# Performance work log

Hardware: AMD Instinct MI355X
Metric: run time of the kernel (lower is better)

## Reference

```python
import jax, jax.numpy as jnp
import numpy as np

D_MODEL = 1024
N_HEADS = 16
D_K = D_MODEL // N_HEADS
D_FF = 4096
THETA = 10000.0
B, S = 2, 2048
EPS = 1e-5


def _trunc_normal(key, shape, fan_in, fan_out):
    std = np.sqrt(2.0 / (fan_in + fan_out))
    return std * jax.random.truncated_normal(key, -3.0, 3.0, shape, dtype=jnp.float32)


def setup_inputs() -> dict:
    key = jax.random.key(0)
    ks = jax.random.split(key, 9)
    x = jax.random.normal(ks[0], (B, S, D_MODEL), dtype=jnp.float32)
    wq = _trunc_normal(ks[1], (D_MODEL, D_MODEL), D_MODEL, D_MODEL)
    wk = _trunc_normal(ks[2], (D_MODEL, D_MODEL), D_MODEL, D_MODEL)
    wv = _trunc_normal(ks[3], (D_MODEL, D_MODEL), D_MODEL, D_MODEL)
    wo = _trunc_normal(ks[4], (D_MODEL, D_MODEL), D_MODEL, D_MODEL)
    w1 = _trunc_normal(ks[5], (D_FF, D_MODEL), D_MODEL, D_FF)
    w2 = _trunc_normal(ks[6], (D_MODEL, D_FF), D_FF, D_MODEL)
    w3 = _trunc_normal(ks[7], (D_FF, D_MODEL), D_MODEL, D_FF)
    g1 = jnp.ones((D_MODEL,), dtype=jnp.float32)
    g2 = jnp.ones((D_MODEL,), dtype=jnp.float32)
    return {"x": x, "wq": wq, "wk": wk, "wv": wv, "wo": wo,
            "w1": w1, "w2": w2, "w3": w3, "g1": g1, "g2": g2}


def _rmsnorm(x, gain):
    xf = x.astype(jnp.float32)
    rms = jnp.sqrt(jnp.mean(xf * xf, axis=-1, keepdims=True) + EPS)
    return (xf / rms * gain).astype(x.dtype)


def _rope(x):
    # x: [B, H, S, D_K]; block-diag 2x2 rotations on consecutive pairs
    s, d = x.shape[-2], x.shape[-1]
    pos = jnp.arange(s, dtype=jnp.float32)  # [S]
    k = jnp.arange(d // 2, dtype=jnp.float32)
    ang = pos[:, None] / (THETA ** (2.0 * k / d))[None, :]  # [S, d/2]
    cos, sin = jnp.cos(ang), jnp.sin(ang)
    xp = x.reshape(*x.shape[:-1], d // 2, 2)
    x0, x1 = xp[..., 0], xp[..., 1]
    r0 = cos * x0 - sin * x1
    r1 = sin * x0 + cos * x1
    return jnp.stack([r0, r1], axis=-1).reshape(x.shape)


def reference(x, wq, wk, wv, wo, w1, w2, w3, g1, g2):
    # --- attention sublayer ---
    h = _rmsnorm(x, g1)
    q = h @ wq.T
    k = h @ wk.T
    v = h @ wv.T
    def split_heads(t):
        b, s, _ = t.shape
        return t.reshape(b, s, N_HEADS, D_K).transpose(0, 2, 1, 3)  # [B,H,S,Dk]
    q, k, v = split_heads(q), split_heads(k), split_heads(v)
    q, k = _rope(q), _rope(k)
    scores = jnp.einsum('bhqd,bhkd->bhqk', q, k) / jnp.sqrt(jnp.float32(D_K))
    s = x.shape[-2]
    causal = jnp.tril(jnp.ones((s, s), dtype=bool))
    scores = jnp.where(causal, scores, -jnp.inf)
    attn = jax.nn.softmax(scores, axis=-1)
    o = jnp.einsum('bhqk,bhkd->bhqd', attn, v)
    o = o.transpose(0, 2, 1, 3).reshape(x.shape[0], s, D_MODEL)
    x = x + o @ wo.T
    # --- SwiGLU FFN sublayer ---
    h2 = _rmsnorm(x, g2)
    a = h2 @ w1.T
    gate = a * jax.nn.sigmoid(a)
    ff = (gate * (h2 @ w3.T)) @ w2.T
    return x + ff
```

## Files before the change

### kernel.cpp

```cpp
#include <hip/hip_runtime.h>
#include <hip/hip_bf16.h>
#include <cstddef>
#include <cstdint>

#define D_MODEL 1024
#define N_HEADS 16
#define D_K     64
#define D_FF    4096
#define BATCH   2
#define SEQ     2048
#define TOKENS  (BATCH * SEQ)
#define EPS     1e-5f

typedef __attribute__((ext_vector_type(8))) short short8;
typedef __attribute__((ext_vector_type(4))) float f32x4;

#define MFMA_BF16 __builtin_amdgcn_mfma_f32_16x16x32_bf16

static __device__ __forceinline__ short f2bf(float f) {
    __hip_bfloat16 h = __float2bfloat16(f);
    short s;
    __builtin_memcpy(&s, &h, 2);
    return s;
}
static __device__ __forceinline__ float bf2f(short s) {
    __hip_bfloat16 h;
    __builtin_memcpy(&h, &s, 2);
    return __bfloat162float(h);
}

static __device__ __forceinline__ void async_ld16(const short* g, short* l) {
    __builtin_amdgcn_global_load_lds(
        (const __attribute__((address_space(1))) void*)g,
        (__attribute__((address_space(3))) void*)l,
        16, 0, 0);
}

__global__ __launch_bounds__(256) void prep_kernel(
    const float* wq, const float* wk, const float* wv, const float* wo,
    const float* w1, const float* w3, const float* w2, short* dst,
    const float* x, const float* g1, __hip_bfloat16* h)
{
    if (blockIdx.x < 16384) {
        const size_t M1 = 1 << 20;
        size_t e = ((size_t)blockIdx.x * 256 + threadIdx.x) * 4;
        const float* src;
        size_t off;
        if (e < M1)            { src = wq; off = e; }
        else if (e < 2 * M1)   { src = wk; off = e - M1; }
        else if (e < 3 * M1)   { src = wv; off = e - 2 * M1; }
        else if (e < 4 * M1)   { src = wo; off = e - 3 * M1; }
        else if (e < 12 * M1) {
            size_t r = (e - 4 * M1) >> 10;
            size_t col = e & 1023;
            size_t p = r >> 5, half = (r >> 4) & 1, idx = r & 15;
            src = half ? w3 : w1;
            off = (p * 16 + idx) * 1024 + col;
        }
        else                   { src = w2; off = e - 12 * M1; }
        float4 v = *reinterpret_cast<const float4*>(src + off);
        short4 o;
        o.x = f2bf(v.x); o.y = f2bf(v.y); o.z = f2bf(v.z); o.w = f2bf(v.w);
        *reinterpret_cast<short4*>(dst + e) = o;
    } else {
        int row = blockIdx.x - 16384;
        int tid = threadIdx.x;
        int lane = tid & 63, wave = tid >> 6;
        const float4* xv = reinterpret_cast<const float4*>(x + (size_t)row * D_MODEL);
        float4 v = xv[tid];
        float ss = v.x * v.x + v.y * v.y + v.z * v.z + v.w * v.w;
#pragma unroll
        for (int m = 1; m < 64; m <<= 1) ss += __shfl_xor(ss, m, 64);
        __shared__ float red[4];
        if (lane == 0) red[wave] = ss;
        __syncthreads();
        float tot = red[0] + red[1] + red[2] + red[3];
        float inv = 1.0f / sqrtf(tot * (1.0f / D_MODEL) + EPS);
        float4 gv = reinterpret_cast<const float4*>(g1)[tid];
        size_t base = (size_t)row * D_MODEL + (size_t)tid * 4;
        h[base + 0] = __float2bfloat16(v.x * inv * gv.x);
        h[base + 1] = __float2bfloat16(v.y * inv * gv.y);
        h[base + 2] = __float2bfloat16(v.z * inv * gv.z);
        h[base + 3] = __float2bfloat16(v.w * inv * gv.w);
    }
}

__global__ __launch_bounds__(256) void resid_norm_kernel(
    const float* __restrict__ x, const short* __restrict__ P,
    const float* __restrict__ g, float* __restrict__ out,
    __hip_bfloat16* __restrict__ h)
{
    int row = blockIdx.x;
    int tid = threadIdx.x;
    int lane = tid & 63, wave = tid >> 6;
    size_t base = (size_t)row * D_MODEL + (size_t)tid * 4;
    float4 v = *reinterpret_cast<const float4*>(x + base);
    short4 p0 = *reinterpret_cast<const short4*>(P + base);
    short4 p1 = *reinterpret_cast<const short4*>(P + (size_t)TOKENS * D_MODEL + base);
    v.x += bf2f(p0.x) + bf2f(p1.x); v.y += bf2f(p0.y) + bf2f(p1.y);
    v.z += bf2f(p0.z) + bf2f(p1.z); v.w += bf2f(p0.w) + bf2f(p1.w);
    *reinterpret_cast<float4*>(out + base) = v;
    float ss = v.x * v.x + v.y * v.y + v.z * v.z + v.w * v.w;
#pragma unroll
    for (int m = 1; m < 64; m <<= 1) ss += __shfl_xor(ss, m, 64);
    __shared__ float red[4];
    if (lane == 0) red[wave] = ss;
    __syncthreads();
    float tot = red[0] + red[1] + red[2] + red[3];
    float inv = 1.0f / sqrtf(tot * (1.0f / D_MODEL) + EPS);
    float4 gv = reinterpret_cast<const float4*>(g)[tid];
    h[base + 0] = __float2bfloat16(v.x * inv * gv.x);
    h[base + 1] = __float2bfloat16(v.y * inv * gv.y);
    h[base + 2] = __float2bfloat16(v.z * inv * gv.z);
    h[base + 3] = __float2bfloat16(v.w * inv * gv.w);
}

__global__ __launch_bounds__(256) void final_add_kernel(
    float* __restrict__ out, const short* __restrict__ Q)
{
    size_t base = ((size_t)blockIdx.x * 256 + threadIdx.x) * 4;
    float4 v = *reinterpret_cast<const float4*>(out + base);
    short4 q0 = *reinterpret_cast<const short4*>(Q + base);
    short4 q1 = *reinterpret_cast<const short4*>(Q + (size_t)TOKENS * D_MODEL + base);
    v.x += bf2f(q0.x) + bf2f(q1.x); v.y += bf2f(q0.y) + bf2f(q1.y);
    v.z += bf2f(q0.z) + bf2f(q1.z); v.w += bf2f(q0.w) + bf2f(q1.w);
    *reinterpret_cast<float4*>(out + base) = v;
}

template<int EPI>
__global__ __launch_bounds__(256) void gemm_bt(
    const short* __restrict__ A, const short* __restrict__ W,
    void* __restrict__ Cout, int K, int lda, int ldc)
{
    __shared__ short Alds[128 * 64];
    __shared__ short Blds[128 * 64];

    const int lane = threadIdx.x & 63;
    const int wv = threadIdx.x >> 6;
    const int quad = lane >> 4, l16 = lane & 15;
    const int wm = wv & 1, wn = wv >> 1;
    const int rowblk = blockIdx.y * 128;
    const int colblk = blockIdx.x * 128;

    const int srow = lane >> 2;
    const int sseg = ((lane & 3) - (lane >> 3)) & 3;
    const short* sA0 = A + (size_t)(rowblk + wv * 16 + srow) * lda + sseg * 8;
    const short* sA1 = A + (size_t)(rowblk + (wv + 4) * 16 + srow) * lda + sseg * 8;
    const short* sB0 = W + (size_t)(colblk + wv * 16 + srow) * (size_t)K + sseg * 8;
    const short* sB1 = W + (size_t)(colblk + (wv + 4) * 16 + srow) * (size_t)K + sseg * 8;
    short* lA0 = &Alds[wv * 512];
    short* lA1 = &Alds[(wv + 4) * 512];
    short* lB0 = &Blds[wv * 512];
    short* lB1 = &Blds[(wv + 4) * 512];

    int aoff[4], boff[4];
#pragma unroll
    for (int i = 0; i < 4; ++i) {
        int tr = wm * 64 + i * 16 + l16;
        aoff[i] = tr * 32 + ((quad + (tr >> 1)) & 3) * 8;
        int tc = wn * 64 + i * 16 + l16;
        boff[i] = tc * 32 + ((quad + (tc >> 1)) & 3) * 8;
    }

    f32x4 acc[4][4];
#pragma unroll
    for (int i = 0; i < 4; ++i)
#pragma unroll
        for (int j = 0; j < 4; ++j)
            acc[i][j] = (f32x4){0.f, 0.f, 0.f, 0.f};

    for (int kk = 0; kk < K; kk += 64) {
        if (kk) __syncthreads();
        async_ld16(sA0 + kk, lA0);
        async_ld16(sA1 + kk, lA1);
        async_ld16(sB0 + kk, lB0);
        async_ld16(sB1 + kk, lB1);
        async_ld16(sA0 + kk + 32, lA0 + 4096);
        async_ld16(sA1 + kk + 32, lA1 + 4096);
        async_ld16(sB0 + kk + 32, lB0 + 4096);
        async_ld16(sB1 + kk + 32, lB1 + 4096);
        __syncthreads();
#pragma unroll
        for (int hf = 0; hf < 2; ++hf) {
            short8 af[4], bf[4];
#pragma unroll
            for (int i = 0; i < 4; ++i)
                af[i] = *reinterpret_cast<const short8*>(&Alds[hf * 4096 + aoff[i]]);
#pragma unroll
            for (int j = 0; j < 4; ++j)
                bf[j] = *reinterpret_cast<const short8*>(&Blds[hf * 4096 + boff[j]]);
#pragma unroll
            for (int i = 0; i < 4; ++i)
#pragma unroll
                for (int j = 0; j < 4; ++j)
                    acc[i][j] = MFMA_BF16(af[i], bf[j], acc[i][j], 0, 0, 0);
        }
    }

    if (EPI == 2) {
#pragma unroll
        for (int i = 0; i < 4; ++i) {
#pragma unroll
            for (int jp = 0; jp < 2; ++jp) {
#pragma unroll
                for (int r = 0; r < 4; ++r) {
                    int row = rowblk + wm * 64 + i * 16 + quad * 4 + r;
                    int col = blockIdx.x * 64 + wn * 32 + jp * 16 + l16;
                    float a = acc[i][2 * jp][r];
                    float b3 = acc[i][2 * jp + 1][r];
                    float gv = a / (1.f + __expf(-a)) * b3;
                    reinterpret_cast<__hip_bfloat16*>(Cout)[(size_t)row * ldc + col] =
                        __float2bfloat16(gv);
                }
            }
        }
    } else {
#pragma unroll
        for (int i = 0; i < 4; ++i) {
#pragma unroll
            for (int j = 0; j < 4; ++j) {
#pragma unroll
                for (int r = 0; r < 4; ++r) {
                    int row = rowblk + wm * 64 + i * 16 + quad * 4 + r;
                    int col = colblk + wn * 64 + j * 16 + l16;
                    size_t idx = (size_t)row * ldc + col;
                    if (EPI == 3)
                        reinterpret_cast<__hip_bfloat16*>(Cout)[idx] =
                            __float2bfloat16(acc[i][j][r]);
                    else
                        reinterpret_cast<float*>(Cout)[idx] = acc[i][j][r];
                }
            }
        }
    }
}

template<int SPLIT>
__global__ __launch_bounds__(256) void gemm_bt_sk(
    const short* __restrict__ A, const short* __restrict__ W,
    short* __restrict__ P, int K, int lda, int ldc)
{
    __shared__ short Alds[128 * 64];
    __shared__ short Blds[128 * 64];

    const int Kc = K / SPLIT;
    const int kbase = blockIdx.z * Kc;
    short* Cout = P + (size_t)blockIdx.z * TOKENS * ldc;

    const int lane = threadIdx.x & 63;
    const int wv = threadIdx.x >> 6;
    const int quad = lane >> 4, l16 = lane & 15;
    const int wm = wv & 1, wn = wv >> 1;
    const int rowblk = blockIdx.y * 128;
    const int colblk = blockIdx.x * 128;

    const int srow = lane >> 2;
    const int sseg = ((lane & 3) - (lane >> 3)) & 3;
    const short* sA0 = A + (size_t)(rowblk + wv * 16 + srow) * lda + kbase + sseg * 8;
    const short* sA1 = A + (size_t)(rowblk + (wv + 4) * 16 + srow) * lda + kbase + sseg * 8;
    const short* sB0 = W + (size_t)(colblk + wv * 16 + srow) * (size_t)K + kbase + sseg * 8;
    const short* sB1 = W + (size_t)(colblk + (wv + 4) * 16 + srow) * (size_t)K + kbase + sseg * 8;
    short* lA0 = &Alds[wv * 512];
    short* lA1 = &Alds[(wv + 4) * 512];
    short* lB0 = &Blds[wv * 512];
    short* lB1 = &Blds[(wv + 4) * 512];

    int aoff[4], boff[4];
#pragma unroll
    for (int i = 0; i < 4; ++i) {
        int tr = wm * 64 + i * 16 + l16;
        aoff[i] = tr * 32 + ((quad + (tr >> 1)) & 3) * 8;
        int tc = wn * 64 + i * 16 + l16;
        boff[i] = tc * 32 + ((quad + (tc >> 1)) & 3) * 8;
    }

    f32x4 acc[4][4];
#pragma unroll
    for (int i = 0; i < 4; ++i)
#pragma unroll
        for (int j = 0; j < 4; ++j)
            acc[i][j] = (f32x4){0.f, 0.f, 0.f, 0.f};

    for (int kk = 0; kk < Kc; kk += 64) {
        if (kk) __syncthreads();
        async_ld16(sA0 + kk, lA0);
        async_ld16(sA1 + kk, lA1);
        async_ld16(sB0 + kk, lB0);
        async_ld16(sB1 + kk, lB1);
        async_ld16(sA0 + kk + 32, lA0 + 4096);
        async_ld16(sA1 + kk + 32, lA1 + 4096);
        async_ld16(sB0 + kk + 32, lB0 + 4096);
        async_ld16(sB1 + kk + 32, lB1 + 4096);
        __syncthreads();
#pragma unroll
        for (int hf = 0; hf < 2; ++hf) {
            short8 af[4], bf[4];
#pragma unroll
            for (int i = 0; i < 4; ++i)
                af[i] = *reinterpret_cast<const short8*>(&Alds[hf * 4096 + aoff[i]]);
#pragma unroll
            for (int j = 0; j < 4; ++j)
                bf[j] = *reinterpret_cast<const short8*>(&Blds[hf * 4096 + boff[j]]);
#pragma unroll
            for (int i = 0; i < 4; ++i)
#pragma unroll
                for (int j = 0; j < 4; ++j)
                    acc[i][j] = MFMA_BF16(af[i], bf[j], acc[i][j], 0, 0, 0);
        }
    }

#pragma unroll
    for (int i = 0; i < 4; ++i) {
#pragma unroll
        for (int j = 0; j < 4; ++j) {
#pragma unroll
            for (int r = 0; r < 4; ++r) {
                int row = rowblk + wm * 64 + i * 16 + quad * 4 + r;
                int col = colblk + wn * 64 + j * 16 + l16;
                Cout[(size_t)row * ldc + col] = f2bf(acc[i][j][r]);
            }
        }
    }
}

__global__ __launch_bounds__(256) void qkv_post_kernel(
    const short* __restrict__ qk,
    __hip_bfloat16* __restrict__ qb, __hip_bfloat16* __restrict__ kb,
    __hip_bfloat16* __restrict__ vt)
{
    __shared__ float tile[64 * 65];
    if (blockIdx.x < 8192) {
        int idx = blockIdx.x * 256 + threadIdx.x;
        int p = idx & 31;
        int h = (idx >> 5) & 15;
        int tok = idx >> 9;
        int s = tok & (SEQ - 1);
        int b = tok >> 11;
        float invf = exp2f((float)p * -(0.03125f * 13.287712379549449f));
        float ang = (float)s * invf;
        float c, sn;
        sincosf(ang, &sn, &c);
        size_t base = (size_t)tok * 3072 + h * 64 + 2 * p;
        float q0 = bf2f(qk[base]),           q1 = bf2f(qk[base + 1]);
        float k0 = bf2f(qk[base + D_MODEL]), k1 = bf2f(qk[base + D_MODEL + 1]);
        float cq = c * 0.125f, sq = sn * 0.125f;
        size_t ob = ((size_t)(b * N_HEADS + h) * SEQ + s) * D_K + 2 * p;
        qb[ob]     = __float2bfloat16(cq * q0 - sq * q1);
        qb[ob + 1] = __float2bfloat16(sq * q0 + cq * q1);
        kb[ob]     = __float2bfloat16(c * k0 - sn * k1);
        kb[ob + 1] = __float2bfloat16(sn * k0 + c * k1);
    } else {
        int bid = blockIdx.x - 8192;
        const int bh = bid >> 5;
        const int s0 = (bid & 31) * 64;
        const int t = threadIdx.x;
        const int r = t >> 4, c4 = (t & 15) * 4;
        const short* src = qk + ((size_t)(bh >> 4) * SEQ + s0) * 3072 + 2048 + (bh & 15) * 64;
#pragma unroll
        for (int p = 0; p < 4; ++p) {
            int s = p * 16 + r;
            short4 v = *reinterpret_cast<const short4*>(src + (size_t)s * 3072 + c4);
            tile[s * 65 + c4 + 0] = bf2f(v.x);
            tile[s * 65 + c4 + 1] = bf2f(v.y);
            tile[s * 65 + c4 + 2] = bf2f(v.z);
            tile[s * 65 + c4 + 3] = bf2f(v.w);
        }
        __syncthreads();
        const int d = t >> 2, sg = (t & 3) * 16;
        __hip_bfloat16* dst = vt + ((size_t)bh * 64 + d) * SEQ + s0 + sg;
        short8 o0, o1;
#pragma unroll
        for (int i = 0; i < 8; ++i) o0[i] = f2bf(tile[(sg + i) * 65 + d]);
#pragma unroll
        for (int i = 0; i < 8; ++i) o1[i] = f2bf(tile[(sg + 8 + i) * 65 + d]);
        *reinterpret_cast<short8*>(dst) = o0;
        *reinterpret_cast<short8*>(dst + 8) = o1;
    }
}

__global__ __launch_bounds__(512) void attn_kernel(
    const __hip_bfloat16* __restrict__ qbp, const __hip_bfloat16* __restrict__ kbp,
    const __hip_bfloat16* __restrict__ vtp, __hip_bfloat16* __restrict__ o)
{
    const int wave = threadIdx.x >> 6;
    const int lane = threadIdx.x & 63;
    const int quad = lane >> 4, l16 = lane & 15;
    const int bh = blockIdx.y;
    const int qt = (wave < 4) ? blockIdx.x : (15 - blockIdx.x);
    const int q0 = qt * 128 + (wave & 3) * 32;
    const int qmax = q0 + 31;

    const short* Q  = reinterpret_cast<const short*>(qbp) + ((size_t)bh * SEQ + q0) * D_K;
    const short* Kg = reinterpret_cast<const short*>(kbp) + (size_t)bh * SEQ * D_K;
    const short* Vg = reinterpret_cast<const short*>(vtp) + (size_t)bh * D_K * SEQ;

    short8 qfr[2][2];
#pragma unroll
    for (int f = 0; f < 2; ++f) {
        qfr[f][0] = *reinterpret_cast<const short8*>(Q + (size_t)(f * 16 + l16) * D_K + quad * 8);
        qfr[f][1] = *reinterpret_cast<const short8*>(Q + (size_t)(f * 16 + l16) * D_K + 32 + quad * 8);
    }

    f32x4 oacc[2][4];
    f32x4 lacc[2];
#pragma unroll
    for (int f = 0; f < 2; ++f) {
        lacc[f] = (f32x4){0.f, 0.f, 0.f, 0.f};
#pragma unroll
        for (int g = 0; g < 4; ++g) oacc[f][g] = (f32x4){0.f, 0.f, 0.f, 0.f};
    }

    short8 ones;
#pragma unroll
    for (int i = 0; i < 8; ++i) ones[i] = (short)0x3F80;

    __shared__ short Kt[64 * 64];
    __shared__ short Vl[64 * 64];
    __shared__ short plds[8][32 * 72];
    short* myP = &plds[wave][0];

    const int srl = lane >> 3;
    const int sp  = lane & 7;
    const int strow = wave * 8 + srl;
    const int sl = (sp - strow) & 7;

    const int ntile = 2 * (15 - blockIdx.x) + 2;
    for (int tile = 0; tile < ntile; ++tile) {
        const int kb0 = tile * 64;
        if (tile) __syncthreads();
        async_ld16(Kg + (size_t)(kb0 + strow) * D_K + sl * 8, &Kt[wave * 512]);
        async_ld16(Vg + (size_t)strow * SEQ + kb0 + sl * 8, &Vl[wave * 512]);
        __syncthreads();

        if (kb0 <= qmax) {
            f32x4 sf[2][4];
#pragma unroll
            for (int kg = 0; kg < 4; ++kg) {
                int row = kg * 16 + l16;
                const short* kr = &Kt[row * 64];
                short8 kf0 = *reinterpret_cast<const short8*>(&kr[((quad + row) & 7) * 8]);
                short8 kf1 = *reinterpret_cast<const short8*>(&kr[((quad + 4 + row) & 7) * 8]);
#pragma unroll
                for (int f = 0; f < 2; ++f) {
                    f32x4 z = (f32x4){0.f, 0.f, 0.f, 0.f};
                    z = MFMA_BF16(qfr[f][0], kf0, z, 0, 0, 0);
                    z = MFMA_BF16(qfr[f][1], kf1, z, 0, 0, 0);
                    sf[f][kg] = z;
                }
            }
#pragma unroll
            for (int f = 0; f < 2; ++f) {
                const int qlo = q0 + f * 16;
#pragma unroll
                for (int kg = 0; kg < 4; ++kg) {
                    const int keylo = kb0 + kg * 16;
                    const bool needmask = keylo >= qlo;
                    const int key = keylo + l16;
#pragma unroll
                    for (int r = 0; r < 4; ++r) {
                        float p = __expf(sf[f][kg][r]);
                        if (needmask) {
                            int qrow = qlo + quad * 4 + r;
                            p = (key > qrow) ? 0.f : p;
                        }
                        myP[(f * 16 + quad * 4 + r) * 72 + kg * 16 + l16] = f2bf(p);
                    }
                }
            }
            asm volatile("s_waitcnt lgkmcnt(0)" ::: "memory");
            short8 pf[2][2];
#pragma unroll
            for (int f = 0; f < 2; ++f) {
#pragma unroll
                for (int hh = 0; hh < 2; ++hh) {
                    pf[f][hh] = *reinterpret_cast<const short8*>(
                        &myP[(f * 16 + l16) * 72 + (hh * 4 + quad) * 8]);
                    lacc[f] = MFMA_BF16(pf[f][hh], ones, lacc[f], 0, 0, 0);
                }
            }
#pragma unroll
            for (int g = 0; g < 4; ++g) {
                int rd = g * 16 + l16;
                const short* vr = &Vl[rd * 64];
                short8 vf0 = *reinterpret_cast<const short8*>(&vr[((quad + rd) & 7) * 8]);
                short8 vf1 = *reinterpret_cast<const short8*>(&vr[((quad + 4 + rd) & 7) * 8]);
#pragma unroll
                for (int f = 0; f < 2; ++f) {
                    oacc[f][g] = MFMA_BF16(pf[f][0], vf0, oacc[f][g], 0, 0, 0);
                    oacc[f][g] = MFMA_BF16(pf[f][1], vf1, oacc[f][g], 0, 0, 0);
                }
            }
        }
    }

    const int b = bh >> 4, h = bh & 15;
#pragma unroll
    for (int f = 0; f < 2; ++f) {
#pragma unroll
        for (int g = 0; g < 4; ++g) {
#pragma unroll
            for (int r = 0; r < 4; ++r) {
                int qrow = q0 + f * 16 + quad * 4 + r;
                float v = oacc[f][g][r] / lacc[f][r];
                o[(size_t)(b * SEQ + qrow) * D_MODEL + h * 64 + g * 16 + l16] =
                    __float2bfloat16(v);
            }
        }
    }
}

extern "C" void kernel_launch(void* const* d_in, const int* in_sizes, int n_in,
                              void* d_out, int out_size, void* d_ws, size_t ws_size,
                              hipStream_t stream)
{
    const float* x  = (const float*)d_in[0];
    const float* wq = (const float*)d_in[1];
    const float* wk = (const float*)d_in[2];
    const float* wv = (const float*)d_in[3];
    const float* wo = (const float*)d_in[4];
    const float* w1 = (const float*)d_in[5];
    const float* w2 = (const float*)d_in[6];
    const float* w3 = (const float*)d_in[7];
    const float* g1 = (const float*)d_in[8];
    const float* g2 = (const float*)d_in[9];
    float* out = (float*)d_out;

    char* ws = (char*)d_ws;
    const size_t OFF_WTS  = 0;
    const size_t OFF_H    = 33554432;
    const size_t OFF_QKV  = 41943040;
    const size_t OFF_QB   = 92274688;
    const size_t OFF_KB   = 100663296;
    const size_t OFF_VT   = 109051904;
    const size_t OFF_O    = 117440512;
    const size_t OFF_P    = OFF_QKV;
    const size_t OFF_GATE = OFF_QKV;
    const size_t OFF_Q2   = OFF_QB;

    short* wts  = (short*)(ws + OFF_WTS);
    short* wqkvb = wts;
    short* wob  = wts + (size_t)3 * (1 << 20);
    short* w13b = wts + (size_t)4 * (1 << 20);
    short* w2b  = wts + (size_t)12 * (1 << 20);
    __hip_bfloat16* h  = (__hip_bfloat16*)(ws + OFF_H);
    short* qkvb = (short*)(ws + OFF_QKV);
    __hip_bfloat16* qb = (__hip_bfloat16*)(ws + OFF_QB);
    __hip_bfloat16* kb = (__hip_bfloat16*)(ws + OFF_KB);
    __hip_bfloat16* vt = (__hip_bfloat16*)(ws + OFF_VT);
    __hip_bfloat16* ob = (__hip_bfloat16*)(ws + OFF_O);
    short* Pwo  = (short*)(ws + OFF_P);
    __hip_bfloat16* gate = (__hip_bfloat16*)(ws + OFF_GATE);
    short* Qw2  = (short*)(ws + OFF_Q2);

    prep_kernel<<<20480, 256, 0, stream>>>(wq, wk, wv, wo, w1, w3, w2, wts, x, g1, h);
    gemm_bt<3><<<dim3(3072 / 128, TOKENS / 128), 256, 0, stream>>>(
        (const short*)h, wqkvb, qkvb, D_MODEL, D_MODEL, 3072);
    qkv_post_kernel<<<9216, 256, 0, stream>>>(qkvb, qb, kb, vt);
    attn_kernel<<<dim3(8, BATCH * N_HEADS), 512, 0, stream>>>(qb, kb, vt, ob);
    gemm_bt_sk<2><<<dim3(D_MODEL / 128, TOKENS / 128, 2), 256, 0, stream>>>(
        (const short*)ob, wob, Pwo, D_MODEL, D_MODEL, D_MODEL);
    resid_norm_kernel<<<TOKENS, 256, 0, stream>>>(x, Pwo, g2, out, h);
    gemm_bt<2><<<dim3(8192 / 128, TOKENS / 128), 256, 0, stream>>>(
        (const short*)h, w13b, gate, D_MODEL, D_MODEL, D_FF);
    gemm_bt_sk<2><<<dim3(D_MODEL / 128, TOKENS / 128, 2), 256, 0, stream>>>(
        (const short*)gate, w2b, Qw2, D_FF, D_FF, D_MODEL);
    final_add_kernel<<<TOKENS * D_MODEL / 1024, 256, 0, stream>>>(out, Qw2);
    (void)in_sizes; (void)n_in; (void)out_size; (void)ws_size;
}
```

Baseline: 377.4 us.

## Shrink attention blocks to two waves and raise split-K for W2 GEMM

```diff
diff --git a/kernel.cpp b/kernel.cpp
--- a/kernel.cpp
+++ b/kernel.cpp
@@ -120,10 +120,13 @@
 {
     size_t base = ((size_t)blockIdx.x * 256 + threadIdx.x) * 4;
     float4 v = *reinterpret_cast<const float4*>(out + base);
-    short4 q0 = *reinterpret_cast<const short4*>(Q + base);
-    short4 q1 = *reinterpret_cast<const short4*>(Q + (size_t)TOKENS * D_MODEL + base);
-    v.x += bf2f(q0.x) + bf2f(q1.x); v.y += bf2f(q0.y) + bf2f(q1.y);
-    v.z += bf2f(q0.z) + bf2f(q1.z); v.w += bf2f(q0.w) + bf2f(q1.w);
+#pragma unroll
+    for (int z = 0; z < 4; ++z) {
+        short4 q = *reinterpret_cast<const short4*>(
+            Q + (size_t)z * TOKENS * D_MODEL + base);
+        v.x += bf2f(q.x); v.y += bf2f(q.y);
+        v.z += bf2f(q.z); v.w += bf2f(q.w);
+    }
     *reinterpret_cast<float4*>(out + base) = v;
 }
 
@@ -378,7 +381,7 @@
     }
 }
 
-__global__ __launch_bounds__(512) void attn_kernel(
+__global__ __launch_bounds__(128) void attn_kernel(
     const __hip_bfloat16* __restrict__ qbp, const __hip_bfloat16* __restrict__ kbp,
     const __hip_bfloat16* __restrict__ vtp, __hip_bfloat16* __restrict__ o)
 {
@@ -386,8 +389,9 @@
     const int lane = threadIdx.x & 63;
     const int quad = lane >> 4, l16 = lane & 15;
     const int bh = blockIdx.y;
-    const int qt = (wave < 4) ? blockIdx.x : (15 - blockIdx.x);
-    const int q0 = qt * 128 + (wave & 3) * 32;
+    const int j = blockIdx.x;
+    const int qt = wave ? (63 - j) : j;
+    const int q0 = qt * 32;
     const int qmax = q0 + 31;
 
     const short* Q  = reinterpret_cast<const short*>(qbp) + ((size_t)bh * SEQ + q0) * D_K;
@@ -416,20 +420,24 @@
 
     __shared__ short Kt[64 * 64];
     __shared__ short Vl[64 * 64];
-    __shared__ short plds[8][32 * 72];
+    __shared__ short plds[2][32 * 72];
     short* myP = &plds[wave][0];
 
     const int srl = lane >> 3;
     const int sp  = lane & 7;
-    const int strow = wave * 8 + srl;
-    const int sl = (sp - strow) & 7;
-
-    const int ntile = 2 * (15 - blockIdx.x) + 2;
+
+    const int ntile = (65 - j) >> 1;
     for (int tile = 0; tile < ntile; ++tile) {
         const int kb0 = tile * 64;
         if (tile) __syncthreads();
-        async_ld16(Kg + (size_t)(kb0 + strow) * D_K + sl * 8, &Kt[wave * 512]);
-        async_ld16(Vg + (size_t)strow * SEQ + kb0 + sl * 8, &Vl[wave * 512]);
+#pragma unroll
+        for (int p = 0; p < 4; ++p) {
+            int r0 = wave * 32 + p * 8;
+            int strow = r0 + srl;
+            int sl = (sp - strow) & 7;
+            async_ld16(Kg + (size_t)(kb0 + strow) * D_K + sl * 8, &Kt[r0 * 64]);
+            async_ld16(Vg + (size_t)strow * SEQ + kb0 + sl * 8, &Vl[r0 * 64]);
+        }
         __syncthreads();
 
         if (kb0 <= qmax) {
@@ -556,13 +564,13 @@
     gemm_bt<3><<<dim3(3072 / 128, TOKENS / 128), 256, 0, stream>>>(
         (const short*)h, wqkvb, qkvb, D_MODEL, D_MODEL, 3072);
     qkv_post_kernel<<<9216, 256, 0, stream>>>(qkvb, qb, kb, vt);
-    attn_kernel<<<dim3(8, BATCH * N_HEADS), 512, 0, stream>>>(qb, kb, vt, ob);
+    attn_kernel<<<dim3(32, BATCH * N_HEADS), 128, 0, stream>>>(qb, kb, vt, ob);
     gemm_bt_sk<2><<<dim3(D_MODEL / 128, TOKENS / 128, 2), 256, 0, stream>>>(
         (const short*)ob, wob, Pwo, D_MODEL, D_MODEL, D_MODEL);
     resid_norm_kernel<<<TOKENS, 256, 0, stream>>>(x, Pwo, g2, out, h);
     gemm_bt<2><<<dim3(8192 / 128, TOKENS / 128), 256, 0, stream>>>(
         (const short*)h, w13b, gate, D_MODEL, D_MODEL, D_FF);
-    gemm_bt_sk<2><<<dim3(D_MODEL / 128, TOKENS / 128, 2), 256, 0, stream>>>(
+    gemm_bt_sk<4><<<dim3(D_MODEL / 128, TOKENS / 128, 4), 256, 0, stream>>>(
         (const short*)gate, w2b, Qw2, D_FF, D_FF, D_MODEL);
     final_add_kernel<<<TOKENS * D_MODEL / 1024, 256, 0, stream>>>(out, Qw2);
     (void)in_sizes; (void)n_in; (void)out_size; (void)ws_size;
```

New measurement: 401.1 us. 6.3% more time.
